# Performance work log

Measured on AMD Instinct MI355X. Metric: run time of the kernel, lower is better.

Reference implementation:

```python
import jax, jax.numpy as jnp
import numpy as np

B, C, P, D = 4096, 1000, 10, 256
N = C * P            # total prototypes
E = 160000           # edges among prototypes
MARGIN = -0.1
LOSS_WEIGHT = 0.1
EPS = 1e-12          # F.normalize eps


def _gcn_conv(x, src, dst, deg_isqrt, w, b):
    # PyG GCNConv: symmetric-normalized aggregation with self-loops (added by caller)
    xw = x @ w                                   # [N, D]
    norm = deg_isqrt[src] * deg_isqrt[dst]       # [E+N]
    msg = norm[:, None] * xw[src]                # [E+N, D]
    out = jax.ops.segment_sum(msg, dst, num_segments=N)
    return out + b


def setup_inputs() -> dict:
    key = jax.random.key(0)
    ks = jax.random.split(key, 8)
    return {
        "hidden": jax.random.normal(ks[0], (B, D), jnp.float32),
        "labels": jax.random.randint(ks[1], (B,), 0, C),
        "edge_index": jax.random.randint(ks[2], (2, E), 0, N),
        "node_features": 0.02 * jax.random.normal(ks[3], (N, D), jnp.float32),
        "w1": jax.random.normal(ks[4], (D, D), jnp.float32) / np.sqrt(D),
        "b1": jnp.zeros((D,), jnp.float32),
        "w2": jax.random.normal(ks[5], (D, D), jnp.float32) / np.sqrt(D),
        "b2": jnp.zeros((D,), jnp.float32),
    }


def reference(hidden, labels, edge_index, node_features, w1, b1, w2, b2):
    # --- PrototypeGCN over the prototype graph (self-loops + sym norm) ---
    loops = jnp.arange(N, dtype=edge_index.dtype)
    src = jnp.concatenate([edge_index[0], loops])
    dst = jnp.concatenate([edge_index[1], loops])
    deg = jax.ops.segment_sum(jnp.ones_like(dst, jnp.float32), dst, num_segments=N)
    deg_isqrt = jnp.where(deg > 0, jax.lax.rsqrt(jnp.maximum(deg, 1.0)), 0.0)
    x = node_features
    x = jax.nn.relu(_gcn_conv(x, src, dst, deg_isqrt, w1, b1))
    x = jax.nn.relu(_gcn_conv(x, src, dst, deg_isqrt, w2, b2))

    # --- cosine similarity, per-class max over prototypes ---
    hidden_norm = hidden / jnp.maximum(jnp.linalg.norm(hidden, axis=1, keepdims=True), EPS)
    proto_norm = x / jnp.maximum(jnp.linalg.norm(x, axis=1, keepdims=True), EPS)
    sim = (1.0 + hidden_norm @ proto_norm.T) / 2.0          # [B, N]
    sim_pc = sim.reshape(B, C, P)
    output = sim_pc.max(axis=2)                              # [B, C]
    topk_idx = sim_pc.argmax(axis=2)                         # [B, C]

    # --- margin-masked cross entropy ---
    ar = jnp.arange(B)
    true_scores = output[ar, labels]
    pred_labels = output.argmax(axis=1)
    pred_scores = output.max(axis=1)
    mask = (true_scores - pred_scores) > MARGIN              # [B] bool
    cnt = mask.sum()
    per_ce = -jax.nn.log_softmax(output, axis=1)[ar, labels]
    ce_loss = jnp.sum(per_ce * mask) / jnp.maximum(cnt, 1).astype(per_ce.dtype)

    # dispersion = -mean(proto_norm @ proto_norm.T) = -||sum_i p_i||^2 / N^2
    s = proto_norm.sum(axis=0)
    dispersion_loss = -(s @ s) / (N * N)
    total_loss = jnp.where(cnt == 0, 0.0, ce_loss + LOSS_WEIGHT * dispersion_loss)

    # --- vectorized usage scatter (replaces Python double loop) ---
    pos_ids = labels * P + topk_idx[ar, labels]
    positive_usage = jnp.zeros((N,), jnp.float32).at[pos_ids].add(1.0)
    wrong = (pred_labels != labels).astype(jnp.float32)
    neg_ids = pred_labels * P + topk_idx[ar, pred_labels]
    negative_usage = jnp.zeros((N,), jnp.float32).at[neg_ids].add(wrong)

    return (output, total_loss, positive_usage, negative_usage)
```

## Files before the change

### kernel.cpp

```cpp
#include <hip/hip_runtime.h>
#include <math.h>

#define B_  4096
#define C_  1000
#define P_  10
#define D_  256
#define N_  10000
#define E_  160000

typedef __attribute__((ext_vector_type(8))) short short8;
typedef __attribute__((ext_vector_type(4))) float floatx4;

__device__ __forceinline__ float waveReduceSum(float v){
  #pragma unroll
  for (int o = 32; o > 0; o >>= 1) v += __shfl_xor(v, o);
  return v;
}
__device__ __forceinline__ unsigned short f2bf(float f){
  unsigned int u = __float_as_uint(f);
  unsigned int r = (u + 0x7FFFu + ((u >> 16) & 1u)) >> 16;
  return (unsigned short)r;
}
__device__ __forceinline__ float bf2f(unsigned short b){
  return __uint_as_float(((unsigned int)b) << 16);
}

__global__ void k_deg_hist(const int* __restrict__ dst, int* __restrict__ deg){
  int e = blockIdx.x * 256 + threadIdx.x;
  if (e < E_) atomicAdd(&deg[dst[e]], 1);
}

__global__ void k_isq(const int* __restrict__ deg, float* __restrict__ isq){
  int n = blockIdx.x * 256 + threadIdx.x;
  if (n < N_) isq[n] = 1.0f / sqrtf((float)(deg[n] + 1));
}

__global__ void k_scatter(const int* __restrict__ src, const int* __restrict__ dst,
                          int* __restrict__ cursor, const float* __restrict__ isq,
                          int* __restrict__ csr_src, float* __restrict__ csr_norm){
  int e = blockIdx.x * 256 + threadIdx.x;
  if (e >= E_) return;
  int d = dst[e], s = src[e];
  int p = atomicAdd(&cursor[d], 1);
  p = (p < 63) ? p : 63;
  csr_src [d * 64 + p] = s;
  csr_norm[d * 64 + p] = isq[s] * isq[d];
}

__global__ void k_split_a(const float* __restrict__ in,
                          unsigned short* __restrict__ hi,
                          unsigned short* __restrict__ lo){
  size_t i = (size_t)blockIdx.x * 256 + threadIdx.x;
  float x = in[i];
  unsigned short h = f2bf(x);
  hi[i] = h;
  lo[i] = f2bf(x - bf2f(h));
}

__global__ void k_split_w(const float* __restrict__ w1, const float* __restrict__ w2,
                          unsigned short* __restrict__ w1h, unsigned short* __restrict__ w1l,
                          unsigned short* __restrict__ w2h, unsigned short* __restrict__ w2l){
  int b = blockIdx.x;
  int k = threadIdx.x;
  const float* w = (b < 256) ? w1 : w2;
  int n = b & 255;
  float x = w[(size_t)k * 256 + n];
  unsigned short h = f2bf(x);
  unsigned short l = f2bf(x - bf2f(h));
  if (b < 256){ w1h[(size_t)n * 256 + k] = h; w1l[(size_t)n * 256 + k] = l; }
  else        { w2h[(size_t)n * 256 + k] = h; w2l[(size_t)n * 256 + k] = l; }
}

__global__ __launch_bounds__(64) void k_gemm_mfma(
    const unsigned short* __restrict__ Ah, const unsigned short* __restrict__ Al,
    const unsigned short* __restrict__ Wh, const unsigned short* __restrict__ Wl,
    float* __restrict__ outp){
  int lane = threadIdx.x;
  int l15 = lane & 15, lq = lane >> 4;
  int rb = blockIdx.x * 64;
  int nb = blockIdx.y * 64;

  floatx4 acc[4][4];
  #pragma unroll
  for (int mt = 0; mt < 4; ++mt)
    #pragma unroll
    for (int nt = 0; nt < 4; ++nt) acc[mt][nt] = (floatx4){0.f,0.f,0.f,0.f};

  int arow[4];
  #pragma unroll
  for (int mt = 0; mt < 4; ++mt){
    int r = rb + mt * 16 + l15;
    arow[mt] = (r < N_) ? r : (N_ - 1);
  }
  for (int kc = 0; kc < 256; kc += 32){
    short8 ah[4], al[4], bh[4], bl[4];
    #pragma unroll
    for (int mt = 0; mt < 4; ++mt){
      size_t o = (size_t)arow[mt] * 256 + kc + lq * 8;
      ah[mt] = *(const short8*)(Ah + o);
      al[mt] = *(const short8*)(Al + o);
    }
    #pragma unroll
    for (int nt = 0; nt < 4; ++nt){
      size_t o = (size_t)(nb + nt * 16 + l15) * 256 + kc + lq * 8;
      bh[nt] = *(const short8*)(Wh + o);
      bl[nt] = *(const short8*)(Wl + o);
    }
    #pragma unroll
    for (int nt = 0; nt < 4; ++nt)
      #pragma unroll
      for (int mt = 0; mt < 4; ++mt){
        floatx4 c = acc[mt][nt];
        c = __builtin_amdgcn_mfma_f32_16x16x32_bf16(al[mt], bh[nt], c, 0, 0, 0);
        c = __builtin_amdgcn_mfma_f32_16x16x32_bf16(ah[mt], bl[nt], c, 0, 0, 0);
        c = __builtin_amdgcn_mfma_f32_16x16x32_bf16(ah[mt], bh[nt], c, 0, 0, 0);
        acc[mt][nt] = c;
      }
  }
  #pragma unroll
  for (int mt = 0; mt < 4; ++mt)
    #pragma unroll
    for (int r = 0; r < 4; ++r){
      int row = rb + mt * 16 + lq * 4 + r;
      if (row < N_){
        #pragma unroll
        for (int nt = 0; nt < 4; ++nt)
          outp[(size_t)row * 256 + nb + nt * 16 + l15] = acc[mt][nt][r];
      }
    }
}

__global__ void k_agg_split(const float* __restrict__ XW, const int* __restrict__ deg,
                            const int* __restrict__ csr_src, const float* __restrict__ csr_norm,
                            const float* __restrict__ isq, const float* __restrict__ bias,
                            unsigned short* __restrict__ Xh, unsigned short* __restrict__ Xl){
  int n    = blockIdx.x * 4 + (threadIdx.x >> 6);
  int lane = threadIdx.x & 63;
  int c4   = lane * 4;
  int   es = csr_src [n * 64 + lane];
  float en = csr_norm[n * 64 + lane];
  int dg = deg[n]; dg = (dg < 64) ? dg : 64;
  float is = isq[n];
  float4 s = *(const float4*)(XW + (size_t)n * 256 + c4);
  float w = is * is;
  float4 a = make_float4(w * s.x, w * s.y, w * s.z, w * s.w);
  int i = 0;
  for (; i + 1 < dg; i += 2){
    int   s0 = __shfl(es, i);     float n0 = __shfl(en, i);
    int   s1 = __shfl(es, i + 1); float n1 = __shfl(en, i + 1);
    float4 v0 = *(const float4*)(XW + (size_t)s0 * 256 + c4);
    float4 v1 = *(const float4*)(XW + (size_t)s1 * 256 + c4);
    a.x += n0 * v0.x; a.y += n0 * v0.y; a.z += n0 * v0.z; a.w += n0 * v0.w;
    a.x += n1 * v1.x; a.y += n1 * v1.y; a.z += n1 * v1.z; a.w += n1 * v1.w;
  }
  if (i < dg){
    int s0 = __shfl(es, i); float n0 = __shfl(en, i);
    float4 v0 = *(const float4*)(XW + (size_t)s0 * 256 + c4);
    a.x += n0 * v0.x; a.y += n0 * v0.y; a.z += n0 * v0.z; a.w += n0 * v0.w;
  }
  float4 b = *(const float4*)(bias + c4);
  float x0 = fmaxf(a.x + b.x, 0.f), x1 = fmaxf(a.y + b.y, 0.f);
  float x2 = fmaxf(a.z + b.z, 0.f), x3 = fmaxf(a.w + b.w, 0.f);
  unsigned short h0 = f2bf(x0), h1 = f2bf(x1), h2 = f2bf(x2), h3 = f2bf(x3);
  ushort4 hv = make_ushort4(h0, h1, h2, h3);
  ushort4 lv = make_ushort4(f2bf(x0 - bf2f(h0)), f2bf(x1 - bf2f(h1)),
                            f2bf(x2 - bf2f(h2)), f2bf(x3 - bf2f(h3)));
  *(ushort4*)(Xh + (size_t)n * 256 + c4) = hv;
  *(ushort4*)(Xl + (size_t)n * 256 + c4) = lv;
}

__global__ void k_agg_norm_split(const float* __restrict__ XW, const int* __restrict__ deg,
                                 const int* __restrict__ csr_src, const float* __restrict__ csr_norm,
                                 const float* __restrict__ isq, const float* __restrict__ bias,
                                 unsigned short* __restrict__ Ph, unsigned short* __restrict__ Pl){
  int n    = blockIdx.x * 4 + (threadIdx.x >> 6);
  int lane = threadIdx.x & 63;
  int c4   = lane * 4;
  int   es = csr_src [n * 64 + lane];
  float en = csr_norm[n * 64 + lane];
  int dg = deg[n]; dg = (dg < 64) ? dg : 64;
  float is = isq[n];
  float4 s = *(const float4*)(XW + (size_t)n * 256 + c4);
  float w = is * is;
  float4 a = make_float4(w * s.x, w * s.y, w * s.z, w * s.w);
  int i = 0;
  for (; i + 1 < dg; i += 2){
    int   s0 = __shfl(es, i);     float n0 = __shfl(en, i);
    int   s1 = __shfl(es, i + 1); float n1 = __shfl(en, i + 1);
    float4 v0 = *(const float4*)(XW + (size_t)s0 * 256 + c4);
    float4 v1 = *(const float4*)(XW + (size_t)s1 * 256 + c4);
    a.x += n0 * v0.x; a.y += n0 * v0.y; a.z += n0 * v0.z; a.w += n0 * v0.w;
    a.x += n1 * v1.x; a.y += n1 * v1.y; a.z += n1 * v1.z; a.w += n1 * v1.w;
  }
  if (i < dg){
    int s0 = __shfl(es, i); float n0 = __shfl(en, i);
    float4 v0 = *(const float4*)(XW + (size_t)s0 * 256 + c4);
    a.x += n0 * v0.x; a.y += n0 * v0.y; a.z += n0 * v0.z; a.w += n0 * v0.w;
  }
  float4 b = *(const float4*)(bias + c4);
  float x0 = fmaxf(a.x + b.x, 0.f), x1 = fmaxf(a.y + b.y, 0.f);
  float x2 = fmaxf(a.z + b.z, 0.f), x3 = fmaxf(a.w + b.w, 0.f);
  float ss = x0*x0 + x1*x1 + x2*x2 + x3*x3;
  float tot = waveReduceSum(ss);
  float nrm = fmaxf(sqrtf(tot), 1e-12f);
  x0 /= nrm; x1 /= nrm; x2 /= nrm; x3 /= nrm;
  unsigned short h0 = f2bf(x0), h1 = f2bf(x1), h2 = f2bf(x2), h3 = f2bf(x3);
  ushort4 hv = make_ushort4(h0, h1, h2, h3);
  ushort4 lv = make_ushort4(f2bf(x0 - bf2f(h0)), f2bf(x1 - bf2f(h1)),
                            f2bf(x2 - bf2f(h2)), f2bf(x3 - bf2f(h3)));
  *(ushort4*)(Ph + (size_t)n * 256 + c4) = hv;
  *(ushort4*)(Pl + (size_t)n * 256 + c4) = lv;
}

__global__ void k_norm_split(const float* __restrict__ in,
                             unsigned short* __restrict__ hi,
                             unsigned short* __restrict__ lo){
  int r = blockIdx.x, t = threadIdx.x;
  float v = in[(size_t)r * 256 + t];
  float ss = waveReduceSum(v * v);
  __shared__ float red[4];
  int w = t >> 6;
  if ((t & 63) == 0) red[w] = ss;
  __syncthreads();
  float tot = red[0] + red[1] + red[2] + red[3];
  float nrm = fmaxf(sqrtf(tot), 1e-12f);
  float x = v / nrm;
  unsigned short h = f2bf(x);
  unsigned short l = f2bf(x - bf2f(h));
  hi[(size_t)r * 256 + t] = h;
  lo[(size_t)r * 256 + t] = l;
}

__global__ void k_colsum(const unsigned short* __restrict__ hi,
                         const unsigned short* __restrict__ lo,
                         float* __restrict__ s){
  int d = threadIdx.x;
  int r0 = blockIdx.x * 100;
  float acc = 0.f;
  for (int r = r0; r < r0 + 100; ++r)
    acc += bf2f(hi[(size_t)r * 256 + d]) + bf2f(lo[(size_t)r * 256 + d]);
  atomicAdd(&s[d], acc);
}

__global__ __launch_bounds__(256, 2) void k_sim_max(
    const unsigned short* __restrict__ HNh, const unsigned short* __restrict__ HNl,
    const unsigned short* __restrict__ PNh, const unsigned short* __restrict__ PNl,
    float* __restrict__ out, unsigned char* __restrict__ idxb){
  __shared__ unsigned short Bs_h[80 * 40];
  __shared__ unsigned short Bs_l[80 * 40];
  __shared__ float red[4][32 * 81];

  int tid  = threadIdx.x;
  int wid  = tid >> 6;
  int lane = tid & 63;
  int l15  = lane & 15, lq = lane >> 4;
  int rbw  = blockIdx.y * 256 + wid * 64;
  int cb80 = blockIdx.x * 80;

  floatx4 acc[4][5];
  #pragma unroll
  for (int mt = 0; mt < 4; ++mt)
    #pragma unroll
    for (int nt = 0; nt < 5; ++nt) acc[mt][nt] = (floatx4){0.f,0.f,0.f,0.f};

  for (int kc = 0; kc < 256; kc += 32){
    if (kc) __syncthreads();
    for (int f = tid; f < 640; f += 256){
      int dt = f >= 320;
      int f2 = f - (dt ? 320 : 0);
      int row = f2 >> 2, kq = f2 & 3;
      const unsigned short* gp = (dt ? PNl : PNh) + (size_t)(cb80 + row) * 256 + kc + kq * 8;
      uint4 v = *(const uint4*)gp;
      *(uint4*)((dt ? Bs_l : Bs_h) + row * 40 + kq * 8) = v;
    }
    short8 ah[4], al[4];
    #pragma unroll
    for (int mt = 0; mt < 4; ++mt){
      size_t o = (size_t)(rbw + mt * 16 + l15) * 256 + kc + lq * 8;
      ah[mt] = *(const short8*)(HNh + o);
      al[mt] = *(const short8*)(HNl + o);
    }
    __syncthreads();
    short8 bh[5], bl[5];
    #pragma unroll
    for (int nt = 0; nt < 5; ++nt){
      int ro = (nt * 16 + l15) * 40 + lq * 8;
      bh[nt] = *(const short8*)(Bs_h + ro);
      bl[nt] = *(const short8*)(Bs_l + ro);
    }
    #pragma unroll
    for (int nt = 0; nt < 5; ++nt)
      #pragma unroll
      for (int mt = 0; mt < 4; ++mt){
        floatx4 c = acc[mt][nt];
        c = __builtin_amdgcn_mfma_f32_16x16x32_bf16(al[mt], bh[nt], c, 0, 0, 0);
        c = __builtin_amdgcn_mfma_f32_16x16x32_bf16(ah[mt], bl[nt], c, 0, 0, 0);
        c = __builtin_amdgcn_mfma_f32_16x16x32_bf16(ah[mt], bh[nt], c, 0, 0, 0);
        acc[mt][nt] = c;
      }
  }

  float* redw = red[wid];
  #pragma unroll
  for (int h = 0; h < 2; ++h){
    if (h) __syncthreads();
    #pragma unroll
    for (int m2 = 0; m2 < 2; ++m2){
      int mt = h * 2 + m2;
      #pragma unroll
      for (int nt = 0; nt < 5; ++nt)
        #pragma unroll
        for (int r = 0; r < 4; ++r)
          redw[(m2 * 16 + lq * 4 + r) * 81 + nt * 16 + l15] = acc[mt][nt][r];
    }
    int rloc = lane >> 1;
    int c2   = lane & 1;
    const float* basep = redw + rloc * 81 + c2 * 40;
    float vs[4]; int is[4];
    #pragma unroll
    for (int cc = 0; cc < 4; ++cc){
      float m = 0.5f * (1.0f + basep[cc * 10]); int mi = 0;
      #pragma unroll
      for (int p = 1; p < 10; ++p){
        float v = 0.5f * (1.0f + basep[cc * 10 + p]);
        if (v > m){ m = v; mi = p; }
      }
      vs[cc] = m; is[cc] = mi;
    }
    int grow = rbw + h * 32 + rloc;
    int gcol = blockIdx.x * 8 + c2 * 4;
    *(float4*)(out + (size_t)grow * 1000 + gcol) = make_float4(vs[0], vs[1], vs[2], vs[3]);
    uchar4 u4; u4.x = (unsigned char)is[0]; u4.y = (unsigned char)is[1];
    u4.z = (unsigned char)is[2]; u4.w = (unsigned char)is[3];
    *(uchar4*)(idxb + (size_t)grow * 1000 + gcol) = u4;
  }
}

__global__ void k_row_pass(const float* __restrict__ out, const unsigned char* __restrict__ idxb,
                           const int* __restrict__ labels, int* __restrict__ cnt,
                           float* __restrict__ ce_sum, float* __restrict__ pos_usage,
                           float* __restrict__ neg_usage){
  int b = blockIdx.x * 4 + (threadIdx.x >> 6);
  int lane = threadIdx.x & 63;
  const float* row = out + (size_t)b * 1000;
  float m = -INFINITY, s = 0.f; int bi = 0x7fffffff;
  for (int c = lane; c < 1000; c += 64){
    float v = row[c];
    if (v > m){ s = s * expf(m - v) + 1.f; bi = c; m = v; }
    else       s += expf(v - m);
  }
  #pragma unroll
  for (int o = 32; o > 0; o >>= 1){
    float m2 = __shfl_xor(m, o);
    float s2 = __shfl_xor(s, o);
    int   b2 = __shfl_xor(bi, o);
    float M = fmaxf(m, m2);
    s = s * expf(m - M) + s2 * expf(m2 - M);
    if (m2 > m || (m2 == m && b2 < bi)) bi = b2;
    m = M;
  }
  if (lane == 0){
    int lab = labels[b];
    float true_score = row[lab];
    float per_ce = m + logf(s) - true_score;
    bool mask = (true_score - m) > -0.1f;
    if (mask){ atomicAdd(cnt, 1); atomicAdd(ce_sum, per_ce); }
    int pi = idxb[(size_t)b * 1000 + lab];
    atomicAdd(&pos_usage[lab * P_ + pi], 1.f);
    if (bi != lab){
      int ni = idxb[(size_t)b * 1000 + bi];
      atomicAdd(&neg_usage[bi * P_ + ni], 1.f);
    }
  }
}

__global__ void k_finalize(const float* __restrict__ s, const int* __restrict__ cnt,
                           const float* __restrict__ ce_sum, float* __restrict__ loss_out){
  int t = threadIdx.x;
  float v = s[t];
  float ss = waveReduceSum(v * v);
  __shared__ float red[4];
  if ((t & 63) == 0) red[t >> 6] = ss;
  __syncthreads();
  if (t == 0){
    float tot = red[0] + red[1] + red[2] + red[3];
    float disp = -tot / 1.0e8f;
    int c = *cnt;
    float total = (c == 0) ? 0.f
                : (*ce_sum / (float)(c < 1 ? 1 : c) + 0.1f * disp);
    *loss_out = total;
  }
}

extern "C" void kernel_launch(void* const* d_in, const int* in_sizes, int n_in,
                              void* d_out, int out_size, void* d_ws, size_t ws_size,
                              hipStream_t stream){
  const float* hidden = (const float*)d_in[0];
  const int*   labels = (const int*)  d_in[1];
  const int*   eidx   = (const int*)  d_in[2];
  const float* nodef  = (const float*)d_in[3];
  const float* w1     = (const float*)d_in[4];
  const float* b1     = (const float*)d_in[5];
  const float* w2     = (const float*)d_in[6];
  const float* b2     = (const float*)d_in[7];

  float* out       = (float*)d_out;
  float* loss_out  = out + (size_t)B_ * C_;
  float* pos_usage = loss_out + 1;
  float* neg_usage = pos_usage + N_;

  const int* srcp = eidx;
  const int* dstp = eidx + E_;

  char* base = (char*)d_ws;
  size_t off = 0;
  auto alloc = [&](size_t bytes) -> char* {
    char* p = base + off;
    off = (off + bytes + 255) & ~(size_t)255;
    return p;
  };
  int*   deg_cnt = (int*)  alloc((size_t)N_ * 4);
  int*   cursor  = (int*)  alloc((size_t)N_ * 4);
  float* svec    = (float*)alloc(256 * 4);
  int*   cnt     = (int*)  alloc(4);
  float* ce_sum  = (float*)alloc(4);
  size_t zero_bytes = off;
  float* deg_isqrt = (float*)alloc((size_t)N_ * 4);
  int*   csr_src   = (int*)  alloc((size_t)N_ * 64 * 4);
  float* csr_norm  = (float*)alloc((size_t)N_ * 64 * 4);
  float* XW        = (float*)alloc((size_t)N_ * 256 * 4);
  unsigned short* Xh = (unsigned short*)alloc((size_t)N_ * 256 * 2);
  unsigned short* Xl = (unsigned short*)alloc((size_t)N_ * 256 * 2);
  unsigned short* W1h = (unsigned short*)alloc(256 * 256 * 2);
  unsigned short* W1l = (unsigned short*)alloc(256 * 256 * 2);
  unsigned short* W2h = (unsigned short*)alloc(256 * 256 * 2);
  unsigned short* W2l = (unsigned short*)alloc(256 * 256 * 2);
  unsigned short* HNh = (unsigned short*)alloc((size_t)B_ * 256 * 2);
  unsigned short* HNl = (unsigned short*)alloc((size_t)B_ * 256 * 2);
  unsigned char* idxb = (unsigned char*)alloc((size_t)B_ * C_);

  hipMemsetAsync(base, 0, zero_bytes, stream);
  hipMemsetAsync(loss_out, 0, (size_t)(1 + 2 * N_) * 4, stream);

  k_deg_hist<<<(E_ + 255) / 256, 256, 0, stream>>>(dstp, deg_cnt);
  k_isq<<<(N_ + 255) / 256, 256, 0, stream>>>(deg_cnt, deg_isqrt);
  k_scatter<<<(E_ + 255) / 256, 256, 0, stream>>>(srcp, dstp, cursor, deg_isqrt, csr_src, csr_norm);

  k_split_a<<<N_, 256, 0, stream>>>(nodef, Xh, Xl);
  k_split_w<<<512, 256, 0, stream>>>(w1, w2, W1h, W1l, W2h, W2l);

  dim3 ggrid(157, 4);
  k_gemm_mfma<<<ggrid, 64, 0, stream>>>(Xh, Xl, W1h, W1l, XW);
  k_agg_split<<<N_ / 4, 256, 0, stream>>>(XW, deg_cnt, csr_src, csr_norm, deg_isqrt, b1, Xh, Xl);
  k_gemm_mfma<<<ggrid, 64, 0, stream>>>(Xh, Xl, W2h, W2l, XW);
  k_agg_norm_split<<<N_ / 4, 256, 0, stream>>>(XW, deg_cnt, csr_src, csr_norm, deg_isqrt, b2, Xh, Xl);

  k_norm_split<<<B_, 256, 0, stream>>>(hidden, HNh, HNl);
  k_colsum<<<100, 256, 0, stream>>>(Xh, Xl, svec);

  dim3 sgrid(125, 16);
  k_sim_max<<<sgrid, 256, 0, stream>>>(HNh, HNl, Xh, Xl, out, idxb);

  k_row_pass<<<B_ / 4, 256, 0, stream>>>(out, idxb, labels, cnt, ce_sum, pos_usage, neg_usage);
  k_finalize<<<1, 256, 0, stream>>>(svec, cnt, ce_sum, loss_out);
}
```

Baseline: 370.6 us.

## Double-buffer sim_max tiles, shrink its LDS for occupancy, narrow GEMM tiles

k_sim_max now keeps the prototype tile in one 25.6 KB shared buffer that is split into two halves and alternated across k-chunks. This removes the top-of-loop barrier. The same memory is reused for a per-16-row max reduction, with launch bounds raised to allow 5 blocks per CU. The GCN GEMM uses 64x32 tiles over a doubled grid for more parallelism and less register pressure, and the aggregation loops are unrolled by four to keep more gathers in flight. The costs are extra global stores of narrower float2/byte outputs and more GEMM blocks re-reading A.

```diff
diff --git a/kernel.cpp b/kernel.cpp
--- a/kernel.cpp
+++ b/kernel.cpp
@@ -78,13 +78,13 @@
   int lane = threadIdx.x;
   int l15 = lane & 15, lq = lane >> 4;
   int rb = blockIdx.x * 64;
-  int nb = blockIdx.y * 64;
-
-  floatx4 acc[4][4];
+  int nb = blockIdx.y * 32;
+
+  floatx4 acc[4][2];
   #pragma unroll
   for (int mt = 0; mt < 4; ++mt)
     #pragma unroll
-    for (int nt = 0; nt < 4; ++nt) acc[mt][nt] = (floatx4){0.f,0.f,0.f,0.f};
+    for (int nt = 0; nt < 2; ++nt) acc[mt][nt] = (floatx4){0.f,0.f,0.f,0.f};
 
   int arow[4];
   #pragma unroll
@@ -93,7 +93,7 @@
     arow[mt] = (r < N_) ? r : (N_ - 1);
   }
   for (int kc = 0; kc < 256; kc += 32){
-    short8 ah[4], al[4], bh[4], bl[4];
+    short8 ah[4], al[4], bh[2], bl[2];
     #pragma unroll
     for (int mt = 0; mt < 4; ++mt){
       size_t o = (size_t)arow[mt] * 256 + kc + lq * 8;
@@ -101,13 +101,13 @@
       al[mt] = *(const short8*)(Al + o);
     }
     #pragma unroll
-    for (int nt = 0; nt < 4; ++nt){
+    for (int nt = 0; nt < 2; ++nt){
       size_t o = (size_t)(nb + nt * 16 + l15) * 256 + kc + lq * 8;
       bh[nt] = *(const short8*)(Wh + o);
       bl[nt] = *(const short8*)(Wl + o);
     }
     #pragma unroll
-    for (int nt = 0; nt < 4; ++nt)
+    for (int nt = 0; nt < 2; ++nt)
       #pragma unroll
       for (int mt = 0; mt < 4; ++mt){
         floatx4 c = acc[mt][nt];
@@ -124,7 +124,7 @@
       int row = rb + mt * 16 + lq * 4 + r;
       if (row < N_){
         #pragma unroll
-        for (int nt = 0; nt < 4; ++nt)
+        for (int nt = 0; nt < 2; ++nt)
           outp[(size_t)row * 256 + nb + nt * 16 + l15] = acc[mt][nt][r];
       }
     }
@@ -145,15 +145,19 @@
   float w = is * is;
   float4 a = make_float4(w * s.x, w * s.y, w * s.z, w * s.w);
   int i = 0;
-  for (; i + 1 < dg; i += 2){
-    int   s0 = __shfl(es, i);     float n0 = __shfl(en, i);
-    int   s1 = __shfl(es, i + 1); float n1 = __shfl(en, i + 1);
+  for (; i + 3 < dg; i += 4){
+    int s0 = __shfl(es, i),   s1 = __shfl(es, i+1), s2 = __shfl(es, i+2), s3 = __shfl(es, i+3);
+    float n0 = __shfl(en, i), n1 = __shfl(en, i+1), n2 = __shfl(en, i+2), n3 = __shfl(en, i+3);
     float4 v0 = *(const float4*)(XW + (size_t)s0 * 256 + c4);
     float4 v1 = *(const float4*)(XW + (size_t)s1 * 256 + c4);
-    a.x += n0 * v0.x; a.y += n0 * v0.y; a.z += n0 * v0.z; a.w += n0 * v0.w;
-    a.x += n1 * v1.x; a.y += n1 * v1.y; a.z += n1 * v1.z; a.w += n1 * v1.w;
-  }
-  if (i < dg){
+    float4 v2 = *(const float4*)(XW + (size_t)s2 * 256 + c4);
+    float4 v3 = *(const float4*)(XW + (size_t)s3 * 256 + c4);
+    a.x += n0*v0.x + n1*v1.x + n2*v2.x + n3*v3.x;
+    a.y += n0*v0.y + n1*v1.y + n2*v2.y + n3*v3.y;
+    a.z += n0*v0.z + n1*v1.z + n2*v2.z + n3*v3.z;
+    a.w += n0*v0.w + n1*v1.w + n2*v2.w + n3*v3.w;
+  }
+  for (; i < dg; ++i){
     int s0 = __shfl(es, i); float n0 = __shfl(en, i);
     float4 v0 = *(const float4*)(XW + (size_t)s0 * 256 + c4);
     a.x += n0 * v0.x; a.y += n0 * v0.y; a.z += n0 * v0.z; a.w += n0 * v0.w;
@@ -184,15 +188,19 @@
   float w = is * is;
   float4 a = make_float4(w * s.x, w * s.y, w * s.z, w * s.w);
   int i = 0;
-  for (; i + 1 < dg; i += 2){
-    int   s0 = __shfl(es, i);     float n0 = __shfl(en, i);
-    int   s1 = __shfl(es, i + 1); float n1 = __shfl(en, i + 1);
+  for (; i + 3 < dg; i += 4){
+    int s0 = __shfl(es, i),   s1 = __shfl(es, i+1), s2 = __shfl(es, i+2), s3 = __shfl(es, i+3);
+    float n0 = __shfl(en, i), n1 = __shfl(en, i+1), n2 = __shfl(en, i+2), n3 = __shfl(en, i+3);
     float4 v0 = *(const float4*)(XW + (size_t)s0 * 256 + c4);
     float4 v1 = *(const float4*)(XW + (size_t)s1 * 256 + c4);
-    a.x += n0 * v0.x; a.y += n0 * v0.y; a.z += n0 * v0.z; a.w += n0 * v0.w;
-    a.x += n1 * v1.x; a.y += n1 * v1.y; a.z += n1 * v1.z; a.w += n1 * v1.w;
-  }
-  if (i < dg){
+    float4 v2 = *(const float4*)(XW + (size_t)s2 * 256 + c4);
+    float4 v3 = *(const float4*)(XW + (size_t)s3 * 256 + c4);
+    a.x += n0*v0.x + n1*v1.x + n2*v2.x + n3*v3.x;
+    a.y += n0*v0.y + n1*v1.y + n2*v2.y + n3*v3.y;
+    a.z += n0*v0.z + n1*v1.z + n2*v2.z + n3*v3.z;
+    a.w += n0*v0.w + n1*v1.w + n2*v2.w + n3*v3.w;
+  }
+  for (; i < dg; ++i){
     int s0 = __shfl(es, i); float n0 = __shfl(en, i);
     float4 v0 = *(const float4*)(XW + (size_t)s0 * 256 + c4);
     a.x += n0 * v0.x; a.y += n0 * v0.y; a.z += n0 * v0.z; a.w += n0 * v0.w;
@@ -242,13 +250,11 @@
   atomicAdd(&s[d], acc);
 }
 
-__global__ __launch_bounds__(256, 2) void k_sim_max(
+__global__ __launch_bounds__(256, 5) void k_sim_max(
     const unsigned short* __restrict__ HNh, const unsigned short* __restrict__ HNl,
     const unsigned short* __restrict__ PNh, const unsigned short* __restrict__ PNl,
     float* __restrict__ out, unsigned char* __restrict__ idxb){
-  __shared__ unsigned short Bs_h[80 * 40];
-  __shared__ unsigned short Bs_l[80 * 40];
-  __shared__ float red[4][32 * 81];
+  __shared__ __align__(16) char smem[25600];
 
   int tid  = threadIdx.x;
   int wid  = tid >> 6;
@@ -263,15 +269,17 @@
     #pragma unroll
     for (int nt = 0; nt < 5; ++nt) acc[mt][nt] = (floatx4){0.f,0.f,0.f,0.f};
 
+  int pbuf = 0;
   for (int kc = 0; kc < 256; kc += 32){
-    if (kc) __syncthreads();
+    unsigned short* Bh = (unsigned short*)(smem + pbuf * 12800);
+    unsigned short* Bl = Bh + 3200;
     for (int f = tid; f < 640; f += 256){
       int dt = f >= 320;
       int f2 = f - (dt ? 320 : 0);
       int row = f2 >> 2, kq = f2 & 3;
       const unsigned short* gp = (dt ? PNl : PNh) + (size_t)(cb80 + row) * 256 + kc + kq * 8;
       uint4 v = *(const uint4*)gp;
-      *(uint4*)((dt ? Bs_l : Bs_h) + row * 40 + kq * 8) = v;
+      *(uint4*)((dt ? Bl : Bh) + row * 40 + kq * 8) = v;
     }
     short8 ah[4], al[4];
     #pragma unroll
@@ -285,8 +293,8 @@
     #pragma unroll
     for (int nt = 0; nt < 5; ++nt){
       int ro = (nt * 16 + l15) * 40 + lq * 8;
-      bh[nt] = *(const short8*)(Bs_h + ro);
-      bl[nt] = *(const short8*)(Bs_l + ro);
+      bh[nt] = *(const short8*)(Bh + ro);
+      bl[nt] = *(const short8*)(Bl + ro);
     }
     #pragma unroll
     for (int nt = 0; nt < 5; ++nt)
@@ -298,27 +306,25 @@
         c = __builtin_amdgcn_mfma_f32_16x16x32_bf16(ah[mt], bh[nt], c, 0, 0, 0);
         acc[mt][nt] = c;
       }
-  }
-
-  float* redw = red[wid];
-  #pragma unroll
-  for (int h = 0; h < 2; ++h){
-    if (h) __syncthreads();
-    #pragma unroll
-    for (int m2 = 0; m2 < 2; ++m2){
-      int mt = h * 2 + m2;
+    pbuf ^= 1;
+  }
+
+  __syncthreads();
+
+  float* redw = (float*)smem + wid * 1296;
+  #pragma unroll
+  for (int mt = 0; mt < 4; ++mt){
+    #pragma unroll
+    for (int nt = 0; nt < 5; ++nt)
       #pragma unroll
-      for (int nt = 0; nt < 5; ++nt)
-        #pragma unroll
-        for (int r = 0; r < 4; ++r)
-          redw[(m2 * 16 + lq * 4 + r) * 81 + nt * 16 + l15] = acc[mt][nt][r];
-    }
-    int rloc = lane >> 1;
-    int c2   = lane & 1;
-    const float* basep = redw + rloc * 81 + c2 * 40;
-    float vs[4]; int is[4];
-    #pragma unroll
-    for (int cc = 0; cc < 4; ++cc){
+      for (int r = 0; r < 4; ++r)
+        redw[(lq * 4 + r) * 81 + nt * 16 + l15] = acc[mt][nt][r];
+    int row = lane >> 2;
+    int q   = lane & 3;
+    const float* basep = redw + row * 81 + q * 20;
+    float vs[2]; int is[2];
+    #pragma unroll
+    for (int cc = 0; cc < 2; ++cc){
       float m = 0.5f * (1.0f + basep[cc * 10]); int mi = 0;
       #pragma unroll
       for (int p = 1; p < 10; ++p){
@@ -327,12 +333,11 @@
       }
       vs[cc] = m; is[cc] = mi;
     }
-    int grow = rbw + h * 32 + rloc;
-    int gcol = blockIdx.x * 8 + c2 * 4;
-    *(float4*)(out + (size_t)grow * 1000 + gcol) = make_float4(vs[0], vs[1], vs[2], vs[3]);
-    uchar4 u4; u4.x = (unsigned char)is[0]; u4.y = (unsigned char)is[1];
-    u4.z = (unsigned char)is[2]; u4.w = (unsigned char)is[3];
-    *(uchar4*)(idxb + (size_t)grow * 1000 + gcol) = u4;
+    int grow = rbw + mt * 16 + row;
+    int gcol = blockIdx.x * 8 + q * 2;
+    *(float2*)(out + (size_t)grow * 1000 + gcol) = make_float2(vs[0], vs[1]);
+    idxb[(size_t)grow * 1000 + gcol]     = (unsigned char)is[0];
+    idxb[(size_t)grow * 1000 + gcol + 1] = (unsigned char)is[1];
   }
 }
 
@@ -449,7 +454,7 @@
   k_split_a<<<N_, 256, 0, stream>>>(nodef, Xh, Xl);
   k_split_w<<<512, 256, 0, stream>>>(w1, w2, W1h, W1l, W2h, W2l);
 
-  dim3 ggrid(157, 4);
+  dim3 ggrid(157, 8);
   k_gemm_mfma<<<ggrid, 64, 0, stream>>>(Xh, Xl, W1h, W1l, XW);
   k_agg_split<<<N_ / 4, 256, 0, stream>>>(XW, deg_cnt, csr_src, csr_norm, deg_isqrt, b1, Xh, Xl);
   k_gemm_mfma<<<ggrid, 64, 0, stream>>>(Xh, Xl, W2h, W2l, XW);
```

Result: slower. 604.0 us (+63.0%).
